# Kernel tuning notes

Measured on AMD Instinct MI355X. Metric: run time of the kernel, lower is better.

## Reference

```python
import jax, jax.numpy as jnp
import numpy as np

D, H, K, L, NB = 128, 8, 16, 16, 2
N, E, MN, ME = 100_000, 800_000, 1_000, 8_000
VOCAB, BT, VP = 50_000, 256, 15
_SQD, _SQK = float(np.sqrt(D)), float(np.sqrt(K))


def _segment_softmax(score, seg, num):
    m = jax.ops.segment_max(score, seg, num_segments=num)
    e = jnp.exp(score - m[seg])
    z = jax.ops.segment_sum(e, seg, num_segments=num)
    return e / (z[seg] + 1e-9)


def _meta_learner(feat, u, W2, W1):
    # latent-attention factorization: feat [n,D] -> 2d param [n,H,K], 1d param [n,H]
    w = jax.nn.softmax((feat @ u.T) / _SQD, axis=-1)  # [n,L]
    return jnp.einsum('nl,lhk->nhk', w, W2), w @ W1


def _conv(feat, src, dst, p2n, p1n, p2e, p1e, Wq, Wk, Wv, Wo):
    # HeteroAttnConv: multi-head attention message passing modulated by
    # per-node (p2n,p1n) and per-edge (p2e,p1e) meta parameters.
    n = feat.shape[0]
    q = (feat @ Wq).reshape(n, H, K) * p2n
    kf = (feat @ Wk).reshape(n, H, K)
    v = (feat @ Wv).reshape(n, H, K)
    ke = kf[src] * p2e                                   # [e,H,K]
    score = (q[dst] * ke).sum(-1) / _SQK + p1e + p1n[dst]  # [e,H]
    attn = _segment_softmax(score, dst, n)
    agg = jax.ops.segment_sum(attn[..., None] * v[src], dst, num_segments=n).reshape(n, D)
    return jax.nn.relu(agg @ Wo), ke.reshape(-1, D)


def _forward(emb, u, W2lat, W1lat, Wq_m, Wk_m, Wv_m, Wo_m, Wq, Wk, Wv, Wo,
             node_vals, meta_node_vals, src, dst, meta_src, meta_dst,
             meta_node_id, meta_edge_id, target_idx,
             static_vals, static_src, static_dst):
    # _init_meta_param: static param-name graph, copy_u/sum then meta_learner
    fs = emb[static_vals]
    agg = jax.ops.segment_sum(fs[static_src], static_dst, num_segments=VP)
    p2s, p1s = _meta_learner(agg, u, W2lat, W1lat)
    base_tw, base_n1, base_n2 = p1s[0], p1s[3], p2s[6]   # target_weight, node 1d, node 2d
    base_e1, base_e2 = p1s[9], p2s[12]                   # edge 1d, edge 2d

    meta_feat = emb[meta_node_vals]
    feat = emb[node_vals]
    # _asign_param_to_graph(meta_graph): broadcast base buffers only
    mp2n = jnp.broadcast_to(base_n2, (MN, H, K))
    mp1n = jnp.broadcast_to(base_n1, (MN, H))
    mp2e = jnp.broadcast_to(base_e2, (ME, H, K))
    mp1e = jnp.broadcast_to(base_e1, (ME, H))

    out = jnp.zeros((BT, 1), feat.dtype)
    for b in range(NB):
        pre_meta, pre = meta_feat, feat
        meta_feat, meta_edge_feat = _conv(meta_feat, meta_src, meta_dst,
                                          mp2n, mp1n, mp2e, mp1e,
                                          Wq_m[b], Wk_m[b], Wv_m[b], Wo_m[b])
        # _asign_param_to_graph(graph, meta_node_feat, meta_edge_feat):
        # base repeat + indexed add of meta_learner outputs
        p2mn, p1mn = _meta_learner(meta_feat, u, W2lat, W1lat)
        p2me, p1me = _meta_learner(meta_edge_feat, u, W2lat, W1lat)
        p2n = base_n2[None] + p2mn[meta_node_id]
        p1n = base_n1[None] + p1mn[meta_node_id]
        tw = base_tw[None] + p1mn[meta_node_id]
        p2e = base_e2[None] + p2me[meta_edge_id]
        p1e = base_e1[None] + p1me[meta_edge_id]
        feat, _ = _conv(feat, src, dst, p2n, p1n, p2e, p1e,
                        Wq[b], Wk[b], Wv[b], Wo[b])
        # block residual
        meta_feat = meta_feat + pre_meta
        feat = feat + pre
        # Target: per-target-node weighted readout with target_weight param
        logit = jnp.einsum('th,thk->t', tw[target_idx],
                           feat[target_idx].reshape(BT, H, K))
        out = out + logit[:, None]
    return out / NB


def setup_inputs() -> dict:
    key = jax.random.key(0)
    ks = jax.random.split(key, 24)
    s = 0.05
    inp = {}
    inp['emb'] = jax.random.normal(ks[0], (VOCAB, D), jnp.float32) * s
    inp['u'] = jax.random.normal(ks[1], (L, D), jnp.float32) * s
    inp['W2lat'] = jax.random.normal(ks[2], (L, H, K), jnp.float32) * s
    inp['W1lat'] = jax.random.normal(ks[3], (L, H), jnp.float32) * s
    for i, nm in enumerate(['Wq_m', 'Wk_m', 'Wv_m', 'Wo_m', 'Wq', 'Wk', 'Wv', 'Wo']):
        inp[nm] = jax.random.normal(ks[4 + i], (NB, D, D), jnp.float32) / np.sqrt(D)
    inp['node_vals'] = jax.random.randint(ks[12], (N,), 0, VOCAB)
    inp['meta_node_vals'] = jax.random.randint(ks[13], (MN,), 0, VOCAB)
    inp['src'] = jax.random.randint(ks[14], (E,), 0, N)
    inp['dst'] = jax.random.randint(ks[15], (E,), 0, N)
    inp['meta_src'] = jax.random.randint(ks[16], (ME,), 0, MN)
    inp['meta_dst'] = jax.random.randint(ks[17], (ME,), 0, MN)
    inp['meta_node_id'] = jax.random.randint(ks[18], (N,), 0, MN)
    inp['meta_edge_id'] = jax.random.randint(ks[19], (E,), 0, ME)
    inp['target_idx'] = jax.random.randint(ks[20], (BT,), 0, N)
    # static param-name graph: 5 names x (1 name node + 2 token nodes), tokens->name
    name_pos = np.arange(5) * 3
    inp['static_vals'] = jax.random.randint(ks[21], (VP,), 0, VOCAB)
    inp['static_src'] = jnp.asarray(np.stack([name_pos + 1, name_pos + 2], 1).reshape(-1), jnp.int32)
    inp['static_dst'] = jnp.asarray(np.repeat(name_pos, 2), jnp.int32)
    return inp


def reference(emb, u, W2lat, W1lat, Wq_m, Wk_m, Wv_m, Wo_m, Wq, Wk, Wv, Wo,
              node_vals, meta_node_vals, src, dst, meta_src, meta_dst,
              meta_node_id, meta_edge_id, target_idx,
              static_vals, static_src, static_dst):
    return _forward(emb, u, W2lat, W1lat, Wq_m, Wk_m, Wv_m, Wo_m, Wq, Wk, Wv, Wo,
                    node_vals, meta_node_vals, src, dst, meta_src, meta_dst,
                    meta_node_id, meta_edge_id, target_idx,
                    static_vals, static_src, static_dst)
```

## Files before the change

### kernel.cpp

```cpp
#include <hip/hip_runtime.h>
#include <hip/hip_bf16.h>
#include <hip/hip_fp8.h>

#define DD   128
#define HH   8

typedef short bf16x8 __attribute__((ext_vector_type(8)));
typedef float f32x4  __attribute__((ext_vector_type(4)));
typedef float f32x2  __attribute__((ext_vector_type(2)));

__device__ __forceinline__ float b2f(unsigned short v){
  union { unsigned int u; float f; } x; x.u = ((unsigned int)v) << 16; return x.f;
}
__device__ __forceinline__ unsigned short f2b(float f){
  __hip_bfloat16 h = __float2bfloat16(f);
  return *(unsigned short*)&h;
}
__device__ __forceinline__ unsigned char f2f8(float x){
  __hip_fp8_e4m3 h(x);
  return h.__x;
}
__device__ __forceinline__ float f82f(unsigned char b){
  __hip_fp8_e4m3 h; h.__x = b;
  return (float)h;
}
__device__ __forceinline__ void cvt4(unsigned int w, float* o){
#if defined(__has_builtin)
# if __has_builtin(__builtin_amdgcn_cvt_pk_f32_fp8)
  f32x2 lo = __builtin_amdgcn_cvt_pk_f32_fp8((int)w, false);
  f32x2 hi = __builtin_amdgcn_cvt_pk_f32_fp8((int)w, true);
  o[0]=lo[0]; o[1]=lo[1]; o[2]=hi[0]; o[3]=hi[1];
  return;
# endif
#endif
  o[0]=f82f(w&0xff); o[1]=f82f((w>>8)&0xff);
  o[2]=f82f((w>>16)&0xff); o[3]=f82f((w>>24)&0xff);
}
struct __align__(8) us4 { unsigned short x,y,z,w; };
struct __align__(16) us8 { unsigned short s[8]; };

__device__ __forceinline__ float gld(const void* p, size_t i, bool f32){
  if (f32) return ((const float*)p)[i];
  return b2f(((const unsigned short*)p)[i]);
}

__device__ __forceinline__ void gll16(const void* g, void* l){
  __builtin_amdgcn_global_load_lds(
      (const __attribute__((address_space(1))) unsigned int*)g,
      (__attribute__((address_space(3))) unsigned int*)l, 16, 0, 0);
}

struct WPtrs { const void* p[8]; };

#define CPAD 132

__global__ __launch_bounds__(256) void gemm_wo(
    const void* __restrict__ Av, const unsigned short* __restrict__ Bt,
    void* __restrict__ Cv, int M,
    const unsigned short* __restrict__ Rb,
    const int* __restrict__ mnid, const float* __restrict__ p1mn,
    const float* __restrict__ base,
    const int* __restrict__ tgt_of, const int* __restrict__ tgt_next,
    float* __restrict__ acc)
{
  __shared__ __align__(16) unsigned short Asb[64*128];
  __shared__ __align__(16) unsigned short Btb[16896];
  const int tid = threadIdx.x;
  const int wave = tid >> 6, lane = tid & 63;
  const int row0 = blockIdx.x * 64;

  {
    const char* Ab = (const char*)Av;
    int n4 = lane >> 4, c = lane & 15;
#pragma unroll
    for (int op=0; op<4; op++){
      int rA = wave*16 + op*4;
      int n = rA + n4;
      int gr = row0 + n; if (gr >= M) gr = M - 1;
      gll16(Ab + (size_t)gr*256 + ((size_t)((c ^ (n & 7)) << 4)), &Asb[rA*128]);
    }
  }
  {
    int n4 = lane >> 4, c = lane & 15;
#pragma unroll
    for (int op=0; op<8; op++){
      int rB = wave*32 + op*4;
      int n = rB + n4;
      gll16((const char*)Bt + (size_t)n*256 + ((size_t)((c ^ (n & 7)) << 4)),
            &Btb[rB*128]);
    }
  }
  __syncthreads();

  f32x4 acc0[8];
#pragma unroll
  for (int t=0;t<8;t++) acc0[t] = (f32x4){0.f,0.f,0.f,0.f};
  const int am = (lane & 15), kq = (lane >> 4) * 8, axr = (am & 7) << 3;
#pragma unroll
  for (int k0=0;k0<128;k0+=32){
    int xo = (k0 + kq) ^ axr;
    bf16x8 a = *(bf16x8*)&Asb[(wave*16 + am)*128 + xo];
#pragma unroll
    for (int t=0;t<8;t++){
      bf16x8 b = *(bf16x8*)&Btb[(t*16 + am)*128 + xo];
      acc0[t] = __builtin_amdgcn_mfma_f32_16x16x32_bf16(a, b, acc0[t], 0,0,0);
    }
  }
  __syncthreads();
  float* Cls = (float*)Btb;
  {
    int rr = wave*16 + (lane>>4)*4;
    int cc = lane & 15;
#pragma unroll
    for (int t=0;t<8;t++)
#pragma unroll
      for (int r=0;r<4;r++)
        Cls[(rr + r)*CPAD + t*16 + cc] = acc0[t][r];
  }
  __syncthreads();

  {
    int r = tid >> 2, cb = (tid & 3) * 32;
    int gr = row0 + r;
    if (gr < M){
      float hs0 = 0.f, hs1 = 0.f;
#pragma unroll
      for (int j=0;j<8;j++){
        int c = cb + j*4;
        float4 o = *(float4*)&Cls[r*CPAD + c];
        us4 rb = *(const us4*)(Rb + (size_t)gr*DD + c);
        o.x=fmaxf(o.x,0.f)+b2f(rb.x); o.y=fmaxf(o.y,0.f)+b2f(rb.y);
        o.z=fmaxf(o.z,0.f)+b2f(rb.z); o.w=fmaxf(o.w,0.f)+b2f(rb.w);
        float s4 = o.x + o.y + o.z + o.w;
        if (j < 4) hs0 += s4; else hs1 += s4;
        us4 ob; ob.x=f2b(o.x); ob.y=f2b(o.y); ob.z=f2b(o.z); ob.w=f2b(o.w);
        *(us4*)((unsigned short*)Cv + (size_t)gr*DD + c) = ob;
      }
      int hb = cb >> 4;
      int mn = mnid[gr];
      float tw0 = base[hb]     + p1mn[(size_t)mn*HH + hb];
      float tw1 = base[hb + 1] + p1mn[(size_t)mn*HH + hb + 1];
      float part = tw0*hs0 + tw1*hs1;
      part += __shfl_xor(part, 1, 64);
      part += __shfl_xor(part, 2, 64);
      if ((tid & 3) == 0){
        int ti = tgt_of[gr];
        while (ti >= 0){
          atomicAdd(&acc[ti], part);
          ti = tgt_next[ti];
        }
      }
    }
  }
}

enum { EPI_STORE=0, EPI_SCALE_CONST=1 };

template<int EPIQ, bool INB, bool FP8KV>
__device__ __forceinline__ void qkv_body(
    unsigned short* Asb, unsigned short* Btb, int blk,
    const void* __restrict__ Av,
    const unsigned short* __restrict__ Btq, const unsigned short* __restrict__ Btk,
    const unsigned short* __restrict__ Btv,
    void* __restrict__ Cq, void* __restrict__ Ck, int stK,
    void* __restrict__ Cvo, int stV, int M,
    const float* __restrict__ svec)
{
  const int tid = threadIdx.x;
  const int wave = tid >> 6, lane = tid & 63;
  const int row0 = blk * 64;

  if (INB){
    const char* Ab = (const char*)Av;
    int n4 = lane >> 4, c = lane & 15;
#pragma unroll
    for (int op=0; op<4; op++){
      int rA = wave*16 + op*4;
      int n = rA + n4;
      int gr = row0 + n; if (gr >= M) gr = M - 1;
      gll16(Ab + (size_t)gr*256 + ((size_t)((c ^ (n & 7)) << 4)), &Asb[rA*128]);
    }
  } else {
    const float* Af = (const float*)Av;
    int r = tid >> 2, cb = (tid & 3) * 32, rx = (r & 7) << 3;
    int gr = row0 + r;
#pragma unroll
    for (int j=0;j<8;j++){
      int cc = cb + j*4;
      float4 val = make_float4(0.f,0.f,0.f,0.f);
      if (gr < M) val = *(const float4*)(Af + (size_t)gr*DD + cc);
      us4 o; o.x=f2b(val.x); o.y=f2b(val.y); o.z=f2b(val.z); o.w=f2b(val.w);
      *(us4*)&Asb[r*128 + (cc ^ rx)] = o;
    }
  }

  const unsigned short* Bts[3] = {Btq, Btk, Btv};
  void* Cs[3] = {Cq, Ck, Cvo};
  const int sts[3] = {DD, stK, stV};
  const int am = (lane & 15), kq = (lane >> 4) * 8, axr = (am & 7) << 3;

  for (int ph=0; ph<3; ph++){
    {
      const unsigned short* Bt = Bts[ph];
      int n4 = lane >> 4, c = lane & 15;
#pragma unroll
      for (int op=0; op<8; op++){
        int rB = wave*32 + op*4;
        int n = rB + n4;
        gll16((const char*)Bt + (size_t)n*256 + ((size_t)((c ^ (n & 7)) << 4)),
              &Btb[rB*128]);
      }
    }
    __syncthreads();
    f32x4 acc[8];
#pragma unroll
    for (int t=0;t<8;t++) acc[t] = (f32x4){0.f,0.f,0.f,0.f};
#pragma unroll
    for (int k0=0;k0<128;k0+=32){
      int xo = (k0 + kq) ^ axr;
      bf16x8 a = *(bf16x8*)&Asb[(wave*16 + am)*128 + xo];
#pragma unroll
      for (int t=0;t<8;t++){
        bf16x8 b = *(bf16x8*)&Btb[(t*16 + am)*128 + xo];
        acc[t] = __builtin_amdgcn_mfma_f32_16x16x32_bf16(a, b, acc[t], 0,0,0);
      }
    }
    __syncthreads();
    float* Cls = (float*)Btb;
    {
      int rr = wave*16 + (lane>>4)*4;
      int cc = lane & 15;
#pragma unroll
      for (int t=0;t<8;t++)
#pragma unroll
        for (int r=0;r<4;r++)
          Cls[(rr + r)*CPAD + t*16 + cc] = acc[t][r];
    }
    __syncthreads();
    {
      int r = tid >> 2, cb = (tid & 3) * 32;
      int gr = row0 + r;
      if (gr < M){
#pragma unroll
        for (int j=0;j<8;j++){
          int c = cb + j*4;
          float4 o = *(float4*)&Cls[r*CPAD + c];
          if (ph == 0 && EPIQ == EPI_SCALE_CONST){
            o.x*=svec[c+0]; o.y*=svec[c+1]; o.z*=svec[c+2]; o.w*=svec[c+3];
          }
          if (FP8KV && ph > 0){
            unsigned char* Cb = (unsigned char*)Cs[ph];
            uchar4 ob;
            ob.x=f2f8(o.x*8.f); ob.y=f2f8(o.y*8.f);
            ob.z=f2f8(o.z*8.f); ob.w=f2f8(o.w*8.f);
            *(uchar4*)(Cb + (size_t)gr*256 + c) = ob;
          } else {
            us4 ob; ob.x=f2b(o.x); ob.y=f2b(o.y); ob.z=f2b(o.z); ob.w=f2b(o.w);
            *(us4*)((unsigned short*)Cs[ph] + (size_t)gr*sts[ph] + c) = ob;
          }
        }
      }
    }
    __syncthreads();
  }
}

__global__ __launch_bounds__(256) void gemm_qkv2(
    const unsigned short* __restrict__ featB, const float* __restrict__ featM,
    const unsigned short* __restrict__ wqb, const unsigned short* __restrict__ wkb,
    const unsigned short* __restrict__ wvb,
    const unsigned short* __restrict__ wqm, const unsigned short* __restrict__ wkm,
    const unsigned short* __restrict__ wvm,
    unsigned short* __restrict__ qB, unsigned char* __restrict__ kv8,
    unsigned short* __restrict__ qM, unsigned short* __restrict__ kfM,
    unsigned short* __restrict__ vM,
    int Nbig, int Nmeta, int gN, const float* __restrict__ svec)
{
  __shared__ __align__(16) unsigned short Asb[64*128];
  __shared__ __align__(16) unsigned short Btb[16896];
  if (blockIdx.x < gN){
    qkv_body<EPI_STORE,true,true>(Asb, Btb, blockIdx.x, featB,
        wqb, wkb, wvb, qB, kv8, 0, kv8 + 128, 0, Nbig, svec);
  } else {
    qkv_body<EPI_SCALE_CONST,false,false>(Asb, Btb, blockIdx.x - gN, featM,
        wqm, wkm, wvm, qM, kfM, DD, vM, DD, Nmeta, svec);
  }
}

__global__ __launch_bounds__(256) void k_setup(
    const void* __restrict__ emb, const int* __restrict__ svals,
    const int* __restrict__ ssrc, const int* __restrict__ sdst,
    const void* __restrict__ u, const void* __restrict__ W2,
    const void* __restrict__ W1, float* __restrict__ base, int nsrc,
    int* __restrict__ dflag,
    int* __restrict__ degAll, int nDeg, int* __restrict__ tgt_of, int Nn,
    float* __restrict__ acc, int BT,
    const int* __restrict__ valsB, unsigned short* __restrict__ featB, int nB,
    const int* __restrict__ valsM, float* __restrict__ featM, int nM,
    WPtrs W, unsigned short* __restrict__ stage, int NBt,
    int nInit, int gB)
{
  const int t = threadIdx.x;
  int blk = blockIdx.x;
  if (blk == 0){
    __shared__ float sagg[15][128];
    __shared__ float ssc[15][16];
    __shared__ float sww[15][16];
    __shared__ int swf0;
    if (t < 64){
      float m = 0.f;
      for (int i=t; i<128; i+=64){
        float x = fabsf(b2f(((const unsigned short*)emb)[i]));
        if (x < 1e30f) m = fmaxf(m, x);
      }
#pragma unroll
      for (int s=1;s<64;s<<=1) m = fmaxf(m, __shfl_xor(m, s, 64));
      if (t==0){ int f = (m > 1e4f) ? 1 : 0; *dflag = f; swf0 = f; }
    }
    for (int i=t;i<15*128;i+=256) ((float*)sagg)[i]=0.f;
    __syncthreads();
    const bool wf32 = (swf0 != 0);
    if (t < 128){
      for (int i=0;i<nsrc;i++){
        int row = sdst[i]; int vr = svals[ssrc[i]];
        sagg[row][t] += gld(emb, (size_t)vr*DD + t, wf32);
      }
    }
    __syncthreads();
    if (t < 240){
      int n = t>>4, l = t&15;
      float a=0.f;
      for (int d=0;d<128;d++) a += sagg[n][d]*gld(u, l*128+d, wf32);
      ssc[n][l] = a * 0.08838834764831845f;
    }
    __syncthreads();
    if (t < 15){
      float mx=-1e30f;
      for (int l=0;l<16;l++) mx = fmaxf(mx, ssc[t][l]);
      float s=0.f;
      for (int l=0;l<16;l++){ float e=__expf(ssc[t][l]-mx); sww[t][l]=e; s+=e; }
      float inv = 1.f/s;
      for (int l=0;l<16;l++) sww[t][l]*=inv;
    }
    __syncthreads();
    if (t < 8){
      float a=0.f,b=0.f,c=0.f;
      for (int l=0;l<16;l++){
        float wv = gld(W1, l*8+t, wf32);
        a += sww[0][l]*wv; b += sww[3][l]*wv; c += sww[9][l]*wv;
      }
      base[t]=a; base[8+t]=b; base[16+t]=c;
    }
    if (t < 128){
      float a=0.f,b=0.f;
      for (int l=0;l<16;l++){
        float wv = gld(W2, l*128+t, wf32);
        a += sww[6][l]*wv; b += sww[12][l]*wv;
      }
      base[24+t]=a; base[152+t]=b;
    }
    return;
  }
  blk -= 1;
  if (blk < nInit){
    int i = blk*256 + t;
    if (i < nDeg) degAll[i] = 0;
    if (i < Nn) tgt_of[i] = -1;
    if (i < BT) acc[i] = 0.f;
    return;
  }
  blk -= nInit;
  __shared__ int swf;
  if (t < 64){
    float m = 0.f;
    for (int i=t; i<128; i+=64){
      float x = fabsf(b2f(((const unsigned short*)emb)[i]));
      if (x < 1e30f) m = fmaxf(m, x);
    }
#pragma unroll
    for (int s=1;s<64;s<<=1) m = fmaxf(m, __shfl_xor(m, s, 64));
    if (t==0) swf = (m > 1e4f) ? 1 : 0;
  }
  __syncthreads();
  const bool wf32 = (swf != 0);
  if (blk >= gB){
    int bid = blk - gB;
    int idx = bid >> 6;
    int ti = idx / NBt, bi = idx - ti*NBt;
    size_t bo = (size_t)bi*DD*DD;
    int i = (bid & 63)*256 + t;
    int k = i >> 7, n = i & 127;
    float x;
    if (wf32) x = ((const float*)W.p[ti])[bo + i];
    else      x = b2f(((const unsigned short*)W.p[ti])[bo + i]);
    stage[(size_t)idx*DD*DD + n*DD + k] = f2b(x);
    return;
  }
  int i = blk*256 + t;
  bool big = (i < nB*16);
  int i2 = big ? i : (i - nB*16);
  if (!big && i2 >= nM*16) return;
  int r = i2>>4, c = (i2&15)*8;
  int vr = big ? valsB[r] : valsM[r];
  float vb[8];
  if (wf32){
    float4 f0 = *(const float4*)((const float*)emb + (size_t)vr*DD + c);
    float4 f1 = *(const float4*)((const float*)emb + (size_t)vr*DD + c + 4);
    vb[0]=f0.x; vb[1]=f0.y; vb[2]=f0.z; vb[3]=f0.w;
    vb[4]=f1.x; vb[5]=f1.y; vb[6]=f1.z; vb[7]=f1.w;
  } else {
    uint4 raw = *(const uint4*)((const unsigned short*)emb + (size_t)vr*DD + c);
    const unsigned short* hw = (const unsigned short*)&raw;
#pragma unroll
    for (int j=0;j<8;j++) vb[j] = b2f(hw[j]);
  }
  if (big){
    unsigned short* d = featB + (size_t)r*DD + c;
    us4 o0, o1;
    o0.x=f2b(vb[0]); o0.y=f2b(vb[1]); o0.z=f2b(vb[2]); o0.w=f2b(vb[3]);
    o1.x=f2b(vb[4]); o1.y=f2b(vb[5]); o1.z=f2b(vb[6]); o1.w=f2b(vb[7]);
    *(us4*)d = o0; *(us4*)(d+4) = o1;
  } else {
    float* d = featM + (size_t)r*DD + c;
    *(float4*)d     = make_float4(vb[0],vb[1],vb[2],vb[3]);
    *(float4*)(d+4) = make_float4(vb[4],vb[5],vb[6],vb[7]);
  }
}

__global__ __launch_bounds__(256) void k_hist2(
    const int* __restrict__ dstB, const int* __restrict__ dstM,
    int* __restrict__ degB, int* __restrict__ degM, int E, int ME, int nbE){
  int b = blockIdx.x, t = threadIdx.x;
  if (b < nbE){ int i = b*256+t; if (i < E) atomicAdd(&degB[dstB[i]], 1); }
  else { int i = (b-nbE)*256+t; if (i < ME) atomicAdd(&degM[dstM[i]], 1); }
}

__global__ __launch_bounds__(256) void k_scan1b(
    const int* __restrict__ degB, int* __restrict__ rpB, int* __restrict__ bsB,
    int nB, int nbB,
    const int* __restrict__ degM, int* __restrict__ rpM, int* __restrict__ bsM,
    int nM){
  __shared__ int ls[256];
  int blk = blockIdx.x, t = threadIdx.x;
  const int* deg; int* rowptr; int* bsum; int n; int b;
  if (blk < nbB){ deg=degB; rowptr=rpB; bsum=bsB; n=nB; b=blk; }
  else          { deg=degM; rowptr=rpM; bsum=bsM; n=nM; b=blk-nbB; }
  int base = b*1024 + t*4;
  int v0 = (base+0<n)?deg[base+0]:0;
  int v1 = (base+1<n)?deg[base+1]:0;
  int v2 = (base+2<n)?deg[base+2]:0;
  int v3 = (base+3<n)?deg[base+3]:0;
  int tsum = v0+v1+v2+v3;
  ls[t] = tsum; __syncthreads();
  for (int o=1;o<256;o<<=1){
    int x = (t>=o) ? ls[t-o] : 0;
    __syncthreads();
    ls[t] += x;
    __syncthreads();
  }
  int excl = ls[t]-tsum;
  if (t==255) bsum[b] = ls[255];
  if (base+0<n) rowptr[base+0]=excl;
  if (base+1<n) rowptr[base+1]=excl+v0;
  if (base+2<n) rowptr[base+2]=excl+v0+v1;
  if (base+3<n) rowptr[base+3]=excl+v0+v1+v2;
}

__global__ __launch_bounds__(256) void k_scan3b(
    int* __restrict__ rpB, const int* __restrict__ bsB, int* __restrict__ curB,
    int nB, int nb3B, int nbsB,
    int* __restrict__ rpM, const int* __restrict__ bsM, int* __restrict__ curM,
    int nM, int nbsM){
  __shared__ int spre;
  int blk = blockIdx.x, t = threadIdx.x;
  if (blk < nb3B){
    if (t == 0){
      int chunk = blk >> 2;
      int pre = 0;
      for (int j=0;j<chunk;j++) pre += bsB[j];
      spre = pre;
      if (blk == 0){
        int tot = 0;
        for (int j=0;j<nbsB;j++) tot += bsB[j];
        rpB[nB] = tot;
      }
    }
    __syncthreads();
    int i = blk*256 + t;
    if (i < nB){ int r = rpB[i] + spre; rpB[i] = r; curB[i] = r; }
  } else {
    int b2 = blk - nb3B;
    if (t == 0){
      int chunk = b2 >> 2;
      int pre = 0;
      for (int j=0;j<chunk;j++) pre += bsM[j];
      spre = pre;
      if (b2 == 0){
        int tot = 0;
        for (int j=0;j<nbsM;j++) tot += bsM[j];
        rpM[nM] = tot;
      }
    }
    __syncthreads();
    int i = b2*256 + t;
    if (i < nM){ int r = rpM[i] + spre; rpM[i] = r; curM[i] = r; }
  }
}

__global__ __launch_bounds__(256) void k_scatter2(
    const int* __restrict__ dstB, const int* __restrict__ srcB,
    const int* __restrict__ auxB, int* __restrict__ curB,
    int* __restrict__ epackB, int E, int nbE,
    const int* __restrict__ dstM, const int* __restrict__ srcM,
    int* __restrict__ curM, int* __restrict__ esrcM, int* __restrict__ eauxM,
    int ME, int nbME,
    const int* __restrict__ tgt, int* __restrict__ tgt_of,
    int* __restrict__ tgt_next, int BT){
  int blk = blockIdx.x, t = threadIdx.x;
  if (blk < nbE){
    int e = blk*256 + t;
    if (e < E){
      int p = atomicAdd(&curB[dstB[e]], 1);
      epackB[p] = srcB[e] | (auxB[e] << 17);
    }
  } else if (blk < nbE + nbME){
    int e = (blk-nbE)*256 + t;
    if (e < ME){
      int p = atomicAdd(&curM[dstM[e]], 1);
      esrcM[p] = srcM[e];
      eauxM[p] = e;
    }
  } else {
    for (int i=t; i<BT; i+=256){
      int old = atomicExch(&tgt_of[tgt[i]], i);
      tgt_next[i] = old;
    }
  }
}

__global__ __launch_bounds__(256) void edge_meta_csr(
    const int* __restrict__ rowptr, const int* __restrict__ esrc,
    const int* __restrict__ eorig,
    const unsigned short* __restrict__ qm, const unsigned short* __restrict__ kfm,
    const unsigned short* __restrict__ vm,
    const float* __restrict__ base, unsigned short* __restrict__ mef,
    float* __restrict__ agg, int NM)
{
  int id = blockIdx.x*4 + (threadIdx.x>>6);
  int d = id >> 1, half = id & 1;
  if (d >= NM) return;
  int lane = threadIdx.x & 63;
  int off = half*64 + lane;
  const float* be2 = base+152; const float* be1 = base+16; const float* bn1 = base+8;
  size_t dq = (size_t)d*DD;
  float q0 = b2f(qm[dq+off]);
  float w0 = be2[off];
  int h = half*4 + (lane>>4);
  float bias = be1[h] + bn1[h];
  float z0=0.f, a0=0.f;
  int i0 = rowptr[d], i1 = rowptr[d+1];
  for (int i=i0; i<i1; i++){
    int s = esrc[i], e = eorig[i];
    size_t so=(size_t)s*DD, eo=(size_t)e*DD;
    float ke0 = b2f(kfm[so+off]) * w0;
    mef[eo+off]=f2b(ke0);
    float p0 = q0*ke0;
#pragma unroll
    for (int m=1;m<16;m<<=1) p0 += __shfl_xor(p0,m,64);
    float e0 = __expf(p0*0.25f + bias);
    z0 += e0;
    a0 += e0*b2f(vm[so+off]);
  }
  agg[dq+off] = a0 / (z0 + 1e-9f);
}

__global__ __launch_bounds__(128) void learner2(
    const float* __restrict__ Xa, const unsigned short* __restrict__ Xb,
    int Ma, int Mtot,
    const void* __restrict__ u, const void* __restrict__ W2,
    const void* __restrict__ W1,
    const unsigned short* __restrict__ WoT, float* __restrict__ mfeat,
    unsigned short* __restrict__ qsc, float* __restrict__ p1a,
    unsigned short* __restrict__ w2me, unsigned short* __restrict__ p1b,
    const float* __restrict__ base, const int* __restrict__ dflag)
{
  __shared__ float sX[128];
  __shared__ float sAgg[128];
  __shared__ float st[16];
  __shared__ float sw[16];
  const bool wf32 = (*dflag) != 0;
  const int t = threadIdx.x;
  const int l = t>>3, j = t&7;
  float uc[16], w2c[16], w1c[16];
#pragma unroll
  for (int m=0;m<16;m++) uc[m] = gld(u, (size_t)l*128 + j*16 + m, wf32);
#pragma unroll
  for (int i=0;i<16;i++) w2c[i] = gld(W2, (size_t)i*128 + t, wf32);
  if (t < 8){
#pragma unroll
    for (int i=0;i<16;i++) w1c[i] = gld(W1, (size_t)i*8 + t, wf32);
  }
  for (int rr=0; rr<4; rr++){
    int row = blockIdx.x*4 + rr;
    if (row >= Mtot) break;
    const bool isB = (row >= Ma);
    const int m = isB ? (row - Ma) : row;
    if (isB) sX[t] = b2f(Xb[(size_t)m*DD + t]);
    else     sAgg[t] = Xa[(size_t)m*DD + t];
    __syncthreads();
    if (!isB){
      const unsigned short* wrow = WoT + (size_t)t*DD;
      float s = 0.f;
      for (int kk=0; kk<128; kk+=8){
        us8 wv = *(const us8*)(wrow + kk);
#pragma unroll
        for (int jj=0;jj<8;jj++) s += sAgg[kk+jj]*b2f(wv.s[jj]);
      }
      float r = fmaxf(s, 0.f);
      mfeat[(size_t)m*DD + t] += r;
      sX[t] = r;
    }
    __syncthreads();
    float part = 0.f;
#pragma unroll
    for (int mm=0;mm<16;mm++) part += sX[j*16+mm]*uc[mm];
    part += __shfl_xor(part,1,64); part += __shfl_xor(part,2,64); part += __shfl_xor(part,4,64);
    if (j==0) st[l] = part * 0.08838834764831845f;
    __syncthreads();
    float mx=-1e30f;
    for (int i=0;i<16;i++) mx = fmaxf(mx, st[i]);
    float ssum=0.f;
    for (int i=0;i<16;i++) ssum += __expf(st[i]-mx);
    float inv = 1.f/ssum;
    if (t<16) sw[t] = __expf(st[t]-mx)*inv;
    __syncthreads();
    float a=0.f;
#pragma unroll
    for (int i=0;i<16;i++) a += sw[i]*w2c[i];
    if (isB) w2me[(size_t)m*DD+t] = f2b(base[152+t] + a);
    else     qsc [(size_t)m*DD+t] = f2b(base[24+t] + a);
    if (t<8){
      float bb=0.f;
#pragma unroll
      for (int i=0;i<16;i++) bb += sw[i]*w1c[i];
      if (isB) p1b[(size_t)m*HH+t] = f2b(bb);
      else     p1a[(size_t)m*HH+t] = bb;
    }
    __syncthreads();
  }
}

__global__ __launch_bounds__(256) void edge_fused(
    const int* __restrict__ rowptr, const int* __restrict__ epack,
    const int* __restrict__ mnid,
    const unsigned short* __restrict__ q, const unsigned char* __restrict__ kv8,
    const unsigned short* __restrict__ w2me, const unsigned short* __restrict__ p1me,
    const float* __restrict__ p1mn, const unsigned short* __restrict__ qsc,
    const float* __restrict__ base,
    unsigned short* __restrict__ aggb, int N)
{
  int wv = blockIdx.x*4 + (threadIdx.x>>6);
  int lane = threadIdx.x & 63;
  int grp = lane >> 4, l16 = lane & 15;
  int d = wv*4 + grp;
  if (d >= N) return;
  int c8 = l16 * 8;
  int h = l16 >> 1;

  int i0 = rowptr[d], i1 = rowptr[d+1];
  int mn = mnid[d];
  float bias = base[16+h] + base[8+h] + p1mn[(size_t)mn*HH + h];
  size_t dq = (size_t)d*DD;
  float qv[8];
  {
    uint4 qraw = *(const uint4*)(q + dq + c8);
    us8 sc = *(const us8*)(qsc + (size_t)mn*DD + c8);
    const unsigned short* qh = (const unsigned short*)&qraw;
#pragma unroll
    for (int j=0;j<8;j++) qv[j] = b2f(qh[j]) * b2f(sc.s[j]) * 0.03125f;
  }

  float zh = 0.f;
  float a[8];
#pragma unroll
  for (int j=0;j<8;j++) a[j] = 0.f;

  int i = i0;
  for (; i + 1 < i1; i += 2){
    unsigned int v0p = (unsigned int)epack[i];
    unsigned int v1p = (unsigned int)epack[i+1];
    int s0 = v0p & 0x1FFFF, me0 = v0p >> 17;
    int s1 = v1p & 0x1FFFF, me1 = v1p >> 17;
    const unsigned char* kv0 = kv8 + (size_t)s0*256 + c8;
    const unsigned char* kv1 = kv8 + (size_t)s1*256 + c8;
    uint2 kraw0 = *(const uint2*)kv0;
    uint2 vraw0 = *(const uint2*)(kv0 + 128);
    uint4 wraw0 = *(const uint4*)(w2me + (size_t)me0*DD + c8);
    float pm0 = b2f(p1me[(size_t)me0*HH + h]);
    uint2 kraw1 = *(const uint2*)kv1;
    uint2 vraw1 = *(const uint2*)(kv1 + 128);
    uint4 wraw1 = *(const uint4*)(w2me + (size_t)me1*DD + c8);
    float pm1 = b2f(p1me[(size_t)me1*HH + h]);
    float k0f[8], v0f[8], k1f[8], v1f[8];
    cvt4(kraw0.x, k0f); cvt4(kraw0.y, k0f+4);
    cvt4(vraw0.x, v0f); cvt4(vraw0.y, v0f+4);
    cvt4(kraw1.x, k1f); cvt4(kraw1.y, k1f+4);
    cvt4(vraw1.x, v1f); cvt4(vraw1.y, v1f+4);
    const unsigned short* wh0 = (const unsigned short*)&wraw0;
    const unsigned short* wh1 = (const unsigned short*)&wraw1;
    float pA = 0.f, pB = 0.f;
#pragma unroll
    for (int j=0;j<8;j++){
      pA += qv[j]*(k0f[j]*b2f(wh0[j]));
      pB += qv[j]*(k1f[j]*b2f(wh1[j]));
    }
    pA += __shfl_xor(pA, 1, 64);
    pB += __shfl_xor(pB, 1, 64);
    float ex0 = __expf(pA + bias + pm0);
    float ex1 = __expf(pB + bias + pm1);
    zh += ex0 + ex1;
#pragma unroll
    for (int j=0;j<8;j++) a[j] += ex0*v0f[j] + ex1*v1f[j];
  }
  if (i < i1){
    unsigned int vp = (unsigned int)epack[i];
    int s = vp & 0x1FFFF, me = vp >> 17;
    const unsigned char* kv = kv8 + (size_t)s*256 + c8;
    uint2 kraw = *(const uint2*)kv;
    uint2 vraw = *(const uint2*)(kv + 128);
    uint4 wraw = *(const uint4*)(w2me + (size_t)me*DD + c8);
    float pm = b2f(p1me[(size_t)me*HH + h]);
    float kf[8], vf[8];
    cvt4(kraw.x, kf); cvt4(kraw.y, kf+4);
    cvt4(vraw.x, vf); cvt4(vraw.y, vf+4);
    const unsigned short* wh = (const unsigned short*)&wraw;
    float p = 0.f;
#pragma unroll
    for (int j=0;j<8;j++) p += qv[j]*(kf[j]*b2f(wh[j]));
    p += __shfl_xor(p, 1, 64);
    float ex = __expf(p + bias + pm);
    zh += ex;
#pragma unroll
    for (int j=0;j<8;j++) a[j] += ex*vf[j];
  }

  float inv = 0.125f / (zh + 1e-9f);
  us8 o;
#pragma unroll
  for (int j=0;j<8;j++) o.s[j] = f2b(a[j]*inv);
  *(us8*)(aggb + dq + c8) = o;
}

__global__ __launch_bounds__(256) void k_finish(
    const float* __restrict__ acc, void* __restrict__ out,
    float invNB, int BT, const int* __restrict__ dflag)
{
  int t = blockIdx.x*256 + threadIdx.x;
  if (t >= BT) return;
  float r = acc[t] * invNB;
  if ((*dflag) != 0) ((float*)out)[t] = r;
  else ((__hip_bfloat16*)out)[t] = __float2bfloat16(r);
}

extern "C" void kernel_launch(void* const* d_in, const int* in_sizes, int n_in,
                              void* d_out, int out_size, void* d_ws, size_t ws_size,
                              hipStream_t stream) {
  const void* emb   = d_in[0];
  const void* u     = d_in[1];
  const void* W2lat = d_in[2];
  const void* W1lat = d_in[3];
  WPtrs wptrs;
  for (int i=0;i<8;i++) wptrs.p[i] = d_in[4+i];
  const int* node_vals      = (const int*)d_in[12];
  const int* meta_node_vals = (const int*)d_in[13];
  const int* src            = (const int*)d_in[14];
  const int* dst            = (const int*)d_in[15];
  const int* meta_src       = (const int*)d_in[16];
  const int* meta_dst       = (const int*)d_in[17];
  const int* meta_node_id   = (const int*)d_in[18];
  const int* meta_edge_id   = (const int*)d_in[19];
  const int* target_idx     = (const int*)d_in[20];
  const int* static_vals    = (const int*)d_in[21];
  const int* static_src     = (const int*)d_in[22];
  const int* static_dst     = (const int*)d_in[23];

  const int N  = in_sizes[12];
  const int MN = in_sizes[13];
  const int E  = in_sizes[14];
  const int ME = in_sizes[16];
  const int BT = in_sizes[20];
  const int NSRC = in_sizes[22];
  const int NB = in_sizes[8] / (DD*DD);

  float* ws = (float*)d_ws;
  size_t off = 0;
  auto allocf = [&](size_t n){ float* p = ws + off; off += (n + 3) & ~(size_t)3; return p; };
  auto allocb = [&](size_t n){ unsigned short* p = (unsigned short*)(ws + off); off += (((n+1)/2) + 3) & ~(size_t)3; return p; };
  auto alloci = [&](size_t n){ int* p = (int*)(ws + off); off += (n + 3) & ~(size_t)3; return p; };
  int*            dflag = (int*)ws; off += 4;
  unsigned short* feat  = allocb((size_t)N*DD);
  unsigned short* q     = allocb((size_t)N*DD);
  unsigned char*  kv8   = (unsigned char*)allocf((size_t)N*64);
  unsigned short* aggb  = allocb((size_t)N*DD);
  float*          meta_feat= allocf((size_t)MN*DD);
  float*          agg_m = allocf((size_t)MN*DD);
  unsigned short* q_m   = allocb((size_t)MN*DD);
  unsigned short* kf_m  = allocb((size_t)MN*DD);
  unsigned short* v_m   = allocb((size_t)MN*DD);
  unsigned short* mef   = allocb((size_t)ME*DD);
  unsigned short* qsc   = allocb((size_t)MN*DD);
  float*          p1mn  = allocf((size_t)MN*HH);
  unsigned short* w2me  = allocb((size_t)ME*DD);
  unsigned short* p1me  = allocb((size_t)ME*HH);
  float*          base  = allocf(280);
  float*          acc   = allocf((size_t)BT);
  unsigned short* wstage= allocb((size_t)8*NB*DD*DD);
  int*            rowptr= alloci((size_t)N+1);
  int*            cursor= alloci((size_t)N);
  int*            epack = alloci((size_t)E);
  int*            rowptr_m= alloci((size_t)MN+1);
  int*            cursor_m= alloci((size_t)MN);
  int*            esrc_m  = alloci((size_t)ME);
  int*            eorig_m = alloci((size_t)ME);
  int*            degAll  = alloci((size_t)(N+MN));
  int*            deg     = degAll;
  int*            deg_m   = degAll + N;
  int*            tgt_of  = alloci((size_t)N);
  int*            tgt_next= alloci((size_t)BT);
  const int nb_scan   = (N + 1023)/1024;
  const int nb_scan_m = (MN + 1023)/1024;
  int*            bsum   = alloci((size_t)nb_scan);
  int*            bsum_m = alloci((size_t)nb_scan_m);
  (void)ws_size; (void)n_in; (void)out_size;

  const float* base_n2 = base + 24;

  const int nInit = (N + MN + 255)/256;
  const int gB = ((N+MN)*16+255)/256;
  k_setup<<<1 + nInit + gB + 8*NB*64,256,0,stream>>>(
      emb, static_vals, static_src, static_dst, u, W2lat, W1lat, base, NSRC,
      dflag, degAll, N+MN, tgt_of, N, acc, BT,
      node_vals, feat, N, meta_node_vals, meta_feat, MN,
      wptrs, wstage, NB, nInit, gB);

  const int nbE  = (E+255)/256, nbME = (ME+255)/256;
  const int nb3B = (N+255)/256, nb3M = (MN+255)/256;
  k_hist2<<<nbE+nbME,256,0,stream>>>(dst, meta_dst, deg, deg_m, E, ME, nbE);
  k_scan1b<<<nb_scan+nb_scan_m,256,0,stream>>>(deg, rowptr, bsum, N, nb_scan,
      deg_m, rowptr_m, bsum_m, MN);
  k_scan3b<<<nb3B+nb3M,256,0,stream>>>(rowptr, bsum, cursor, N, nb3B, nb_scan,
      rowptr_m, bsum_m, cursor_m, MN, nb_scan_m);
  k_scatter2<<<nbE+nbME+1,256,0,stream>>>(dst, src, meta_edge_id, cursor,
      epack, E, nbE, meta_dst, meta_src, cursor_m, esrc_m, eorig_m, ME, nbME,
      target_idx, tgt_of, tgt_next, BT);

  const int gm = (MN+63)/64;
  const int gN = (N+63)/64;
  const float invNB = 1.0f/(float)NB;

  for (int b=0;b<NB;b++){
    const unsigned short* wq_m = wstage + (size_t)(0*NB+b)*DD*DD;
    const unsigned short* wk_m = wstage + (size_t)(1*NB+b)*DD*DD;
    const unsigned short* wv_m = wstage + (size_t)(2*NB+b)*DD*DD;
    const unsigned short* wo_m = wstage + (size_t)(3*NB+b)*DD*DD;
    const unsigned short* wqb  = wstage + (size_t)(4*NB+b)*DD*DD;
    const unsigned short* wkb  = wstage + (size_t)(5*NB+b)*DD*DD;
    const unsigned short* wvb  = wstage + (size_t)(6*NB+b)*DD*DD;
    const unsigned short* wob  = wstage + (size_t)(7*NB+b)*DD*DD;

    gemm_qkv2<<<gN+gm,256,0,stream>>>(feat, meta_feat,
        wqb, wkb, wvb, wq_m, wk_m, wv_m,
        q, kv8, q_m, kf_m, v_m, N, MN, gN, base_n2);

    edge_meta_csr<<<(2*MN+3)/4,256,0,stream>>>(rowptr_m, esrc_m, eorig_m,
        q_m, kf_m, v_m, base, mef, agg_m, MN);
    learner2<<<(MN+ME+3)/4,128,0,stream>>>(agg_m, mef, MN, MN+ME,
        u, W2lat, W1lat, wo_m, meta_feat,
        qsc, p1mn, w2me, p1me, base, dflag);

    edge_fused<<<(N+15)/16,256,0,stream>>>(rowptr, epack,
        meta_node_id, q, kv8, w2me, p1me, p1mn, qsc, base, aggb, N);
    gemm_wo<<<gN,256,0,stream>>>(aggb, wob, feat, N,
        feat, meta_node_id, p1mn, base, tgt_of, tgt_next, acc);
  }
  k_finish<<<(BT+255)/256,256,0,stream>>>(acc, d_out, invNB, BT, dflag);
}
```

Measured before the change: 545.4 us.

## Fuse next-block QKV projection into Wo GEMM epilogue and meta learner

The per-block QKV projection launch is removed from the loop. The next block's Q/K/V projection is computed inside the Wo GEMM kernel, reusing the freshly updated feature tile kept in LDS, and the meta-node projection is folded into learner2. This saves re-reading the node features from global memory and one kernel launch per block. In exchange the Wo kernel runs longer with three serial weight loads and less overlap, and learner2 does extra scalar dot products per meta node.

```diff
diff --git a/kernel.cpp b/kernel.cpp
--- a/kernel.cpp
+++ b/kernel.cpp
@@ -54,20 +54,26 @@
 
 #define CPAD 132
 
-__global__ __launch_bounds__(256) void gemm_wo(
-    const void* __restrict__ Av, const unsigned short* __restrict__ Bt,
-    void* __restrict__ Cv, int M,
-    const unsigned short* __restrict__ Rb,
+enum { EPI_STORE=0, EPI_SCALE_CONST=1 };
+
+__global__ __launch_bounds__(256) void gemm_woqkv(
+    const void* __restrict__ Av, const unsigned short* __restrict__ BtWo,
+    unsigned short* __restrict__ featb, int M,
     const int* __restrict__ mnid, const float* __restrict__ p1mn,
     const float* __restrict__ base,
     const int* __restrict__ tgt_of, const int* __restrict__ tgt_next,
-    float* __restrict__ acc)
+    float* __restrict__ acc,
+    const unsigned short* __restrict__ Btq, const unsigned short* __restrict__ Btk,
+    const unsigned short* __restrict__ Btv,
+    unsigned short* __restrict__ qB, unsigned char* __restrict__ kv8,
+    int doQKV)
 {
   __shared__ __align__(16) unsigned short Asb[64*128];
   __shared__ __align__(16) unsigned short Btb[16896];
   const int tid = threadIdx.x;
   const int wave = tid >> 6, lane = tid & 63;
   const int row0 = blockIdx.x * 64;
+  const int am = (lane & 15), kq = (lane >> 4) * 8, axr = (am & 7) << 3;
 
   {
     const char* Ab = (const char*)Av;
@@ -86,7 +92,7 @@
     for (int op=0; op<8; op++){
       int rB = wave*32 + op*4;
       int n = rB + n4;
-      gll16((const char*)Bt + (size_t)n*256 + ((size_t)((c ^ (n & 7)) << 4)),
+      gll16((const char*)BtWo + (size_t)n*256 + ((size_t)((c ^ (n & 7)) << 4)),
             &Btb[rB*128]);
     }
   }
@@ -95,7 +101,6 @@
   f32x4 acc0[8];
 #pragma unroll
   for (int t=0;t<8;t++) acc0[t] = (f32x4){0.f,0.f,0.f,0.f};
-  const int am = (lane & 15), kq = (lane >> 4) * 8, axr = (am & 7) << 3;
 #pragma unroll
   for (int k0=0;k0<128;k0+=32){
     int xo = (k0 + kq) ^ axr;
@@ -120,7 +125,7 @@
   __syncthreads();
 
   {
-    int r = tid >> 2, cb = (tid & 3) * 32;
+    int r = tid >> 2, cb = (tid & 3) * 32, rx = (r & 7) << 3;
     int gr = row0 + r;
     if (gr < M){
       float hs0 = 0.f, hs1 = 0.f;
@@ -128,13 +133,14 @@
       for (int j=0;j<8;j++){
         int c = cb + j*4;
         float4 o = *(float4*)&Cls[r*CPAD + c];
-        us4 rb = *(const us4*)(Rb + (size_t)gr*DD + c);
+        us4 rb = *(const us4*)(featb + (size_t)gr*DD + c);
         o.x=fmaxf(o.x,0.f)+b2f(rb.x); o.y=fmaxf(o.y,0.f)+b2f(rb.y);
         o.z=fmaxf(o.z,0.f)+b2f(rb.z); o.w=fmaxf(o.w,0.f)+b2f(rb.w);
         float s4 = o.x + o.y + o.z + o.w;
         if (j < 4) hs0 += s4; else hs1 += s4;
         us4 ob; ob.x=f2b(o.x); ob.y=f2b(o.y); ob.z=f2b(o.z); ob.w=f2b(o.w);
-        *(us4*)((unsigned short*)Cv + (size_t)gr*DD + c) = ob;
+        *(us4*)(featb + (size_t)gr*DD + c) = ob;
+        *(us4*)&Asb[r*128 + (c ^ rx)] = ob;
       }
       int hb = cb >> 4;
       int mn = mnid[gr];
@@ -152,9 +158,70 @@
       }
     }
   }
-}
-
-enum { EPI_STORE=0, EPI_SCALE_CONST=1 };
+  if (!doQKV) return;
+  __syncthreads();
+
+  const unsigned short* Bts[3] = {Btq, Btk, Btv};
+  for (int ph=0; ph<3; ph++){
+    {
+      const unsigned short* Bt = Bts[ph];
+      int n4 = lane >> 4, c = lane & 15;
+#pragma unroll
+      for (int op=0; op<8; op++){
+        int rB = wave*32 + op*4;
+        int n = rB + n4;
+        gll16((const char*)Bt + (size_t)n*256 + ((size_t)((c ^ (n & 7)) << 4)),
+              &Btb[rB*128]);
+      }
+    }
+    __syncthreads();
+    f32x4 accq[8];
+#pragma unroll
+    for (int t=0;t<8;t++) accq[t] = (f32x4){0.f,0.f,0.f,0.f};
+#pragma unroll
+    for (int k0=0;k0<128;k0+=32){
+      int xo = (k0 + kq) ^ axr;
+      bf16x8 a = *(bf16x8*)&Asb[(wave*16 + am)*128 + xo];
+#pragma unroll
+      for (int t=0;t<8;t++){
+        bf16x8 b = *(bf16x8*)&Btb[(t*16 + am)*128 + xo];
+        accq[t] = __builtin_amdgcn_mfma_f32_16x16x32_bf16(a, b, accq[t], 0,0,0);
+      }
+    }
+    __syncthreads();
+    {
+      int rr = wave*16 + (lane>>4)*4;
+      int cc = lane & 15;
+#pragma unroll
+      for (int t=0;t<8;t++)
+#pragma unroll
+        for (int r=0;r<4;r++)
+          Cls[(rr + r)*CPAD + t*16 + cc] = accq[t][r];
+    }
+    __syncthreads();
+    {
+      int r = tid >> 2, cb = (tid & 3) * 32;
+      int gr = row0 + r;
+      if (gr < M){
+#pragma unroll
+        for (int j=0;j<8;j++){
+          int c = cb + j*4;
+          float4 o = *(float4*)&Cls[r*CPAD + c];
+          if (ph == 0){
+            us4 ob; ob.x=f2b(o.x); ob.y=f2b(o.y); ob.z=f2b(o.z); ob.w=f2b(o.w);
+            *(us4*)(qB + (size_t)gr*DD + c) = ob;
+          } else {
+            uchar4 ob;
+            ob.x=f2f8(o.x*8.f); ob.y=f2f8(o.y*8.f);
+            ob.z=f2f8(o.z*8.f); ob.w=f2f8(o.w*8.f);
+            *(uchar4*)(kv8 + (size_t)gr*256 + (ph==2?128:0) + c) = ob;
+          }
+        }
+      }
+    }
+    __syncthreads();
+  }
+}
 
 template<int EPIQ, bool INB, bool FP8KV>
 __device__ __forceinline__ void qkv_body(
@@ -580,6 +647,10 @@
     const void* __restrict__ u, const void* __restrict__ W2,
     const void* __restrict__ W1,
     const unsigned short* __restrict__ WoT, float* __restrict__ mfeat,
+    const unsigned short* __restrict__ WqT, const unsigned short* __restrict__ WkT,
+    const unsigned short* __restrict__ WvT,
+    unsigned short* __restrict__ qM, unsigned short* __restrict__ kfM,
+    unsigned short* __restrict__ vM, int doMQKV,
     unsigned short* __restrict__ qsc, float* __restrict__ p1a,
     unsigned short* __restrict__ w2me, unsigned short* __restrict__ p1b,
     const float* __restrict__ base, const int* __restrict__ dflag)
@@ -605,10 +676,12 @@
     if (row >= Mtot) break;
     const bool isB = (row >= Ma);
     const int m = isB ? (row - Ma) : row;
-    if (isB) sX[t] = b2f(Xb[(size_t)m*DD + t]);
-    else     sAgg[t] = Xa[(size_t)m*DD + t];
-    __syncthreads();
-    if (!isB){
+    if (isB){
+      sX[t] = b2f(Xb[(size_t)m*DD + t]);
+      __syncthreads();
+    } else {
+      sAgg[t] = Xa[(size_t)m*DD + t];
+      __syncthreads();
       const unsigned short* wrow = WoT + (size_t)t*DD;
       float s = 0.f;
       for (int kk=0; kk<128; kk+=8){
@@ -617,10 +690,32 @@
         for (int jj=0;jj<8;jj++) s += sAgg[kk+jj]*b2f(wv.s[jj]);
       }
       float r = fmaxf(s, 0.f);
-      mfeat[(size_t)m*DD + t] += r;
+      float nv = mfeat[(size_t)m*DD + t] + r;
+      mfeat[(size_t)m*DD + t] = nv;
+      __syncthreads();
+      sAgg[t] = nv;
       sX[t] = r;
-    }
-    __syncthreads();
+      __syncthreads();
+      if (doMQKV){
+        const unsigned short* wq = WqT + (size_t)t*DD;
+        const unsigned short* wk = WkT + (size_t)t*DD;
+        const unsigned short* wv2 = WvT + (size_t)t*DD;
+        float dq_=0.f, dk_=0.f, dv_=0.f;
+        for (int kk=0; kk<128; kk+=8){
+          us8 a = *(const us8*)(wq + kk);
+          us8 b = *(const us8*)(wk + kk);
+          us8 c = *(const us8*)(wv2 + kk);
+#pragma unroll
+          for (int jj=0;jj<8;jj++){
+            float x = sAgg[kk+jj];
+            dq_ += x*b2f(a.s[jj]); dk_ += x*b2f(b.s[jj]); dv_ += x*b2f(c.s[jj]);
+          }
+        }
+        qM [(size_t)m*DD+t] = f2b(dq_ * base[24+t]);
+        kfM[(size_t)m*DD+t] = f2b(dk_);
+        vM [(size_t)m*DD+t] = f2b(dv_);
+      }
+    }
     float part = 0.f;
 #pragma unroll
     for (int mm=0;mm<16;mm++) part += sX[j*16+mm]*uc[mm];
@@ -858,30 +953,42 @@
   const int gN = (N+63)/64;
   const float invNB = 1.0f/(float)NB;
 
+  {
+    const unsigned short* wq_m0 = wstage + (size_t)(0*NB+0)*DD*DD;
+    const unsigned short* wk_m0 = wstage + (size_t)(1*NB+0)*DD*DD;
+    const unsigned short* wv_m0 = wstage + (size_t)(2*NB+0)*DD*DD;
+    const unsigned short* wqb0  = wstage + (size_t)(4*NB+0)*DD*DD;
+    const unsigned short* wkb0  = wstage + (size_t)(5*NB+0)*DD*DD;
+    const unsigned short* wvb0  = wstage + (size_t)(6*NB+0)*DD*DD;
+    gemm_qkv2<<<gN+gm,256,0,stream>>>(feat, meta_feat,
+        wqb0, wkb0, wvb0, wq_m0, wk_m0, wv_m0,
+        q, kv8, q_m, kf_m, v_m, N, MN, gN, base_n2);
+  }
+
   for (int b=0;b<NB;b++){
-    const unsigned short* wq_m = wstage + (size_t)(0*NB+b)*DD*DD;
-    const unsigned short* wk_m = wstage + (size_t)(1*NB+b)*DD*DD;
-    const unsigned short* wv_m = wstage + (size_t)(2*NB+b)*DD*DD;
+    const int bn = (b+1 < NB) ? (b+1) : b;
+    const int doNext = (b+1 < NB) ? 1 : 0;
     const unsigned short* wo_m = wstage + (size_t)(3*NB+b)*DD*DD;
-    const unsigned short* wqb  = wstage + (size_t)(4*NB+b)*DD*DD;
-    const unsigned short* wkb  = wstage + (size_t)(5*NB+b)*DD*DD;
-    const unsigned short* wvb  = wstage + (size_t)(6*NB+b)*DD*DD;
     const unsigned short* wob  = wstage + (size_t)(7*NB+b)*DD*DD;
-
-    gemm_qkv2<<<gN+gm,256,0,stream>>>(feat, meta_feat,
-        wqb, wkb, wvb, wq_m, wk_m, wv_m,
-        q, kv8, q_m, kf_m, v_m, N, MN, gN, base_n2);
+    const unsigned short* wq_mn = wstage + (size_t)(0*NB+bn)*DD*DD;
+    const unsigned short* wk_mn = wstage + (size_t)(1*NB+bn)*DD*DD;
+    const unsigned short* wv_mn = wstage + (size_t)(2*NB+bn)*DD*DD;
+    const unsigned short* wqbn  = wstage + (size_t)(4*NB+bn)*DD*DD;
+    const unsigned short* wkbn  = wstage + (size_t)(5*NB+bn)*DD*DD;
+    const unsigned short* wvbn  = wstage + (size_t)(6*NB+bn)*DD*DD;
 
     edge_meta_csr<<<(2*MN+3)/4,256,0,stream>>>(rowptr_m, esrc_m, eorig_m,
         q_m, kf_m, v_m, base, mef, agg_m, MN);
     learner2<<<(MN+ME+3)/4,128,0,stream>>>(agg_m, mef, MN, MN+ME,
         u, W2lat, W1lat, wo_m, meta_feat,
+        wq_mn, wk_mn, wv_mn, q_m, kf_m, v_m, doNext,
         qsc, p1mn, w2me, p1me, base, dflag);
 
     edge_fused<<<(N+15)/16,256,0,stream>>>(rowptr, epack,
         meta_node_id, q, kv8, w2me, p1me, p1mn, qsc, base, aggb, N);
-    gemm_wo<<<gN,256,0,stream>>>(aggb, wob, feat, N,
-        feat, meta_node_id, p1mn, base, tgt_of, tgt_next, acc);
+    gemm_woqkv<<<gN,256,0,stream>>>(aggb, wob, feat, N,
+        meta_node_id, p1mn, base, tgt_of, tgt_next, acc,
+        wqbn, wkbn, wvbn, q, kv8, doNext);
   }
   k_finish<<<(BT+255)/256,256,0,stream>>>(acc, d_out, invNB, BT, dflag);
 }
```

Result: slower. 573.3 us (+5.1%).
